# Performance work log

Hardware: AMD Instinct MI355X
Metric: run time of the kernel (lower is better)

## Reference

```python
import jax, jax.numpy as jnp
import numpy as np


def setup_inputs() -> dict:
    key = jax.random.key(0)
    k1, k2, k3, k4, k5 = jax.random.split(key, 5)
    B, S, IN, OUT = 4, 2048, 4096, 4096
    x = jax.random.normal(k1, (B, S, IN), dtype=jnp.float32)
    # int8-style quantized weight stored as int32 values in [0, 255]
    weight_q = jax.random.randint(k2, (OUT, IN), 0, 255, dtype=jnp.int32)
    weight_zero_point = jax.random.randint(k3, (OUT,), 0, 255, dtype=jnp.int32)
    weight_scale = jax.random.uniform(k4, (OUT,), dtype=jnp.float32) * 0.01 + 1e-4
    bias = jax.random.normal(k5, (OUT,), dtype=jnp.float32)
    return {"x": x, "weight_q": weight_q, "weight_zero_point": weight_zero_point,
            "weight_scale": weight_scale, "bias": bias}


def reference(x, weight_q, weight_zero_point, weight_scale, bias):
    # Decompress (dequantize) the weight: per-output-channel affine int8 quantization
    # w_fp = (w_q - zero_point) * scale   -> shape [out, in]
    w = (weight_q - weight_zero_point[:, None]).astype(jnp.float32) * weight_scale[:, None]
    # F.linear: y = x @ w.T + bias
    return jnp.einsum('bsi,oi->bso', x, w) + bias
```

## Files before the change

kernel.cpp:

```cpp
#include <hip/hip_runtime.h>
#include <hip/hip_bf16.h>
#include <stdint.h>

typedef __attribute__((ext_vector_type(4))) int i32x4;

#define K_TOT 4096
#define N_TOT 4096

__global__ __launch_bounds__(512) void quant_x_kernel(const float4* __restrict__ x4,
                                                      unsigned int* __restrict__ xq_dw,
                                                      float* __restrict__ s_row,
                                                      int* __restrict__ qsum_row) {
    const int wave = threadIdx.x >> 6, lane = threadIdx.x & 63;
    const long row = (long)blockIdx.x * 8 + wave;
    const float4* xr = x4 + row * (K_TOT / 4);

    float4 v[16];
    float amax = 0.f;
#pragma unroll
    for (int i = 0; i < 16; ++i) {
        v[i] = xr[lane + i * 64];
        amax = fmaxf(amax, fmaxf(fmaxf(fabsf(v[i].x), fabsf(v[i].y)),
                                 fmaxf(fabsf(v[i].z), fabsf(v[i].w))));
    }
#pragma unroll
    for (int off = 32; off; off >>= 1) amax = fmaxf(amax, __shfl_xor(amax, off));
    amax = fmaxf(amax, 1e-30f);
    const float inv = 127.0f / amax;

    int qsum = 0;
    unsigned int* out = xq_dw + row * (K_TOT / 4);
#pragma unroll
    for (int i = 0; i < 16; ++i) {
        int q0 = (int)rintf(v[i].x * inv), q1 = (int)rintf(v[i].y * inv);
        int q2 = (int)rintf(v[i].z * inv), q3 = (int)rintf(v[i].w * inv);
        qsum += q0 + q1 + q2 + q3;
        out[lane + i * 64] = (unsigned int)(q0 & 255) | ((unsigned int)(q1 & 255) << 8) |
                             ((unsigned int)(q2 & 255) << 16) | ((unsigned int)(q3 & 255) << 24);
    }
#pragma unroll
    for (int off = 32; off; off >>= 1) qsum += __shfl_xor(qsum, off);
    if (lane == 0) { s_row[row] = amax / 127.0f; qsum_row[row] = qsum; }
}

__global__ void pack_w_kernel(const int4* __restrict__ wq, unsigned int* __restrict__ w8) {
    const long o = blockIdx.x;
    const int4* src = wq + o * (K_TOT / 4);
    unsigned int* dst = w8 + o * (K_TOT / 4);
    for (int t = threadIdx.x; t < K_TOT / 4; t += blockDim.x) {
        int4 q = src[t];
        dst[t] = (unsigned int)((q.x - 128) & 255) | ((unsigned int)((q.y - 128) & 255) << 8) |
                 ((unsigned int)((q.z - 128) & 255) << 16) | ((unsigned int)((q.w - 128) & 255) << 24);
    }
}


template<int MH>
__device__ __forceinline__ void read_a8(i32x4 (&a)[4], const char* Ab, int wr, int fr, int kg) {
    const int sw = (fr >> 1) & 3;
#pragma unroll
    for (int mi = 0; mi < 4; ++mi) {
        const int row = wr * 128 + (MH * 4 + mi) * 16 + fr;
        a[mi] = *(const i32x4*)(Ab + row * 64 + ((kg ^ sw) << 4));
    }
}

template<int NH>
__device__ __forceinline__ void read_b8(i32x4 (&b)[2], const char* Bb, int rb, int fr, int kg) {
    const int sw = (fr >> 1) & 3;
#pragma unroll
    for (int ni = 0; ni < 2; ++ni) {
        const int row = rb + (NH * 2 + ni) * 16 + fr;
        b[ni] = *(const i32x4*)(Bb + row * 64 + ((kg ^ sw) << 4));
    }
}

template<int MH, int NH>
__device__ __forceinline__ void mfma8(i32x4 (&acc)[8][4], i32x4 (&a)[4], i32x4 (&b)[2]) {
    __builtin_amdgcn_s_setprio(1);
#pragma unroll
    for (int mi = 0; mi < 4; ++mi)
#pragma unroll
        for (int ni = 0; ni < 2; ++ni)
            acc[MH * 4 + mi][NH * 2 + ni] = __builtin_amdgcn_mfma_i32_16x16x64_i8(
                a[mi], b[ni], acc[MH * 4 + mi][NH * 2 + ni], 0, 0, 0);
    __builtin_amdgcn_s_setprio(0);
}

#define BAR() __builtin_amdgcn_s_barrier()
#define LGKM0() asm volatile("s_waitcnt lgkmcnt(0)" ::: "memory")
#define VMCNT2() asm volatile("s_waitcnt vmcnt(2)" ::: "memory")
#define VMCNT0() asm volatile("s_waitcnt vmcnt(0)" ::: "memory")

__launch_bounds__(512, 2)
__global__ void gemm256_i8_kernel(const char* __restrict__ Aq,
                                  const char* __restrict__ Bq,
                                  const float* __restrict__ s_row,
                                  const int* __restrict__ qsum_row,
                                  const float* __restrict__ scale,
                                  const int* __restrict__ zp,
                                  const float* __restrict__ bias,
                                  float* __restrict__ C) {
    __shared__ __align__(16) char lds[4][256 * 64];

    const int nbn = N_TOT / 256;
    int bid = blockIdx.x;
    const int nwg = gridDim.x;
    if ((nwg & 7) == 0) {
        const int cpx = nwg >> 3;
        bid = (bid & 7) * cpx + (bid >> 3);
    }
    const int bm = bid / nbn, bn = bid % nbn;

    const int tid = threadIdx.x;
    const int w = tid >> 6, lane = tid & 63;
    const int wr = w >> 2, wc = w & 3;
    const int fr = lane & 15, kg = lane >> 4;
    const int brb = (wc >> 1) * 128 + (wc & 1) * 64;

    const long a_row0 = (long)bm * 256;
    const long b_row0 = (long)bn * 256;

    i32x4 acc[8][4] = {};
    i32x4 afr[4], b0[2], b1[2];

    auto stage = [&](int t, int mat, int half) {
        const char* G = (mat == 0) ? Aq : Bq;
        const long row0 = ((mat == 0) ? a_row0 : b_row0) + half * 128;
        char* lb = &lds[(t & 1) * 2 + mat][half * 8192 + w * 1024];
        const int row = w * 16 + (lane >> 2);
        const int c = (lane & 3) ^ (((half * 128 + row) >> 1) & 3);
        const char* g = G + (row0 + row) * K_TOT + (long)t * 64 + c * 16;
        __builtin_amdgcn_global_load_lds(
            (const __attribute__((address_space(1))) void*)g,
            (__attribute__((address_space(3))) void*)lb, 16, 0, 0);
    };

    const char* Ab0 = &lds[0][0];
    const char* Bb0 = &lds[1][0];
    const char* Ab1 = &lds[2][0];
    const char* Bb1 = &lds[3][0];

    stage(0, 0, 0); stage(0, 0, 1); stage(0, 1, 0); stage(0, 1, 1);
    stage(1, 1, 0); stage(1, 1, 1);
    VMCNT2();
    BAR();

    const int NIT = K_TOT / 128;
#pragma unroll 1
    for (int it = 0; it < NIT; ++it) {
        const bool nl = (it != NIT - 1);
        const int t1 = 2 * it + 1, t2 = 2 * it + 2, t3 = 2 * it + 3;

        read_a8<0>(afr, Ab0, wr, fr, kg);
        read_b8<0>(b0, Bb0, brb, fr, kg);
        stage(t1, 0, 0);
        BAR(); LGKM0();
        mfma8<0, 0>(acc, afr, b0);
        BAR();
        read_b8<1>(b1, Bb0, brb, fr, kg);
        stage(t1, 0, 1);
        BAR(); LGKM0();
        mfma8<0, 1>(acc, afr, b1);
        BAR();
        read_a8<1>(afr, Ab0, wr, fr, kg);
        if (nl) stage(t2, 1, 0);
        BAR(); LGKM0();
        mfma8<1, 1>(acc, afr, b1);
        BAR();
        if (nl) stage(t2, 1, 1);
        BAR();
        mfma8<1, 0>(acc, afr, b0);
        if (nl) { VMCNT2(); } else { VMCNT0(); }
        BAR();

        read_a8<0>(afr, Ab1, wr, fr, kg);
        read_b8<0>(b0, Bb1, brb, fr, kg);
        if (nl) stage(t2, 0, 0);
        BAR(); LGKM0();
        mfma8<0, 0>(acc, afr, b0);
        BAR();
        read_b8<1>(b1, Bb1, brb, fr, kg);
        if (nl) stage(t2, 0, 1);
        BAR(); LGKM0();
        mfma8<0, 1>(acc, afr, b1);
        BAR();
        read_a8<1>(afr, Ab1, wr, fr, kg);
        if (nl) stage(t3, 1, 0);
        BAR(); LGKM0();
        mfma8<1, 1>(acc, afr, b1);
        BAR();
        if (nl) stage(t3, 1, 1);
        BAR();
        mfma8<1, 0>(acc, afr, b0);
        if (nl) { VMCNT2(); }
        BAR();
    }

    float scs[4], c1s[4], bbs[4]; int cols[4];
#pragma unroll
    for (int n = 0; n < 4; ++n) {
        cols[n] = (int)b_row0 + wc * 64 + n * 16 + fr;
        scs[n] = scale[cols[n]];
        c1s[n] = (float)(128 - zp[cols[n]]);
        bbs[n] = bias[cols[n]];
    }
#pragma unroll
    for (int m = 0; m < 8; ++m) {
#pragma unroll
        for (int j = 0; j < 4; ++j) {
            const long r = a_row0 + wr * 128 + m * 16 + kg * 4 + j;
            const float sr = s_row[r];
            const float qs = (float)qsum_row[r];
#pragma unroll
            for (int n = 0; n < 4; ++n)
                C[r * N_TOT + cols[n]] = ((float)acc[m][n][j] + c1s[n] * qs) * (scs[n] * sr) + bbs[n];
        }
    }
}

__global__ void fallback_kernel(const float* __restrict__ x, const int* __restrict__ wq,
                                const int* __restrict__ zp, const float* __restrict__ sc,
                                const float* __restrict__ bs, float* __restrict__ y) {
    __shared__ float xs[32][33];
    __shared__ float ws[32][33];
    int bm = blockIdx.y, bn = blockIdx.x;
    int tid = threadIdx.x;
    int r = tid >> 5, c = tid & 31;
    float acc[4] = {0.f, 0.f, 0.f, 0.f};
    for (int k0 = 0; k0 < K_TOT; k0 += 32) {
        for (int t = tid; t < 32 * 32; t += 256) {
            int rr = t >> 5, cc = t & 31;
            xs[rr][cc] = x[(long)(bm * 32 + rr) * K_TOT + k0 + cc];
            int o = bn * 32 + rr;
            ws[rr][cc] = (float)(wq[(long)o * K_TOT + k0 + cc] - zp[o]);
        }
        __syncthreads();
#pragma unroll
        for (int kk = 0; kk < 32; ++kk) {
            float wv = ws[c][kk];
#pragma unroll
            for (int j = 0; j < 4; ++j) acc[j] += xs[r + 8 * j][kk] * wv;
        }
        __syncthreads();
    }
    int o = bn * 32 + c;
    float s = sc[o], b = bs[o];
#pragma unroll
    for (int j = 0; j < 4; ++j)
        y[(long)(bm * 32 + r + 8 * j) * N_TOT + o] = acc[j] * s + b;
}

extern "C" void kernel_launch(void* const* d_in, const int* in_sizes, int n_in,
                              void* d_out, int out_size, void* d_ws, size_t ws_size,
                              hipStream_t stream) {
    const float* x = (const float*)d_in[0];
    const int* wq = (const int*)d_in[1];
    const int* zp = (const int*)d_in[2];
    const float* sc = (const float*)d_in[3];
    const float* bs = (const float*)d_in[4];
    float* y = (float*)d_out;

    const long M = (long)in_sizes[0] / K_TOT;

    size_t xq_bytes = (size_t)M * K_TOT;
    size_t w8_bytes = (size_t)N_TOT * K_TOT;
    size_t s_bytes = (size_t)M * 4;
    size_t q_bytes = (size_t)M * 4;
    size_t need = xq_bytes + w8_bytes + s_bytes + q_bytes + 256;

    if (ws_size >= need && (M & 255) == 0) {
        char* p = (char*)d_ws;
        char* xq = p;                       p += xq_bytes;
        char* w8 = p;                       p += w8_bytes;
        float* s_row = (float*)p;           p += s_bytes;
        int* qsum_row = (int*)p;

        quant_x_kernel<<<(unsigned)(M / 8), 512, 0, stream>>>(
            (const float4*)x, (unsigned int*)xq, s_row, qsum_row);
        pack_w_kernel<<<N_TOT, 256, 0, stream>>>((const int4*)wq, (unsigned int*)w8);

        dim3 grid((unsigned)((M / 256) * (N_TOT / 256)));
        gemm256_i8_kernel<<<grid, 512, 0, stream>>>(
            xq, w8, s_row, qsum_row, sc, zp, bs, y);
    } else {
        dim3 grid(N_TOT / 32, (unsigned)(M / 32));
        fallback_kernel<<<grid, 256, 0, stream>>>(x, wq, zp, sc, bs, y);
    }
}
```

Baseline: 197.5 us.

## Fuse x-quant and weight-pack kernels; coarsen GEMM main-loop phases

Merges the activation quantization and weight packing into one launch, with block ranges split by index, so one launch and its tail are removed. In the int8 GEMM main loop, each half-tile now issues two B-fragment reads and two stage loads together, then runs 16 MFMAs per barrier-delimited phase instead of 8. This halves the barriers and LGKM waits per K step. It holds more B fragments live at once and changes how load issue interleaves with MFMA work, which may raise register pressure and alter latency hiding.

After: 193.6 us. About the same (-1.9%).

```diff
diff --git a/kernel.cpp b/kernel.cpp
--- a/kernel.cpp
+++ b/kernel.cpp
@@ -7,50 +7,53 @@
 #define K_TOT 4096
 #define N_TOT 4096
 
-__global__ __launch_bounds__(512) void quant_x_kernel(const float4* __restrict__ x4,
-                                                      unsigned int* __restrict__ xq_dw,
-                                                      float* __restrict__ s_row,
-                                                      int* __restrict__ qsum_row) {
+__global__ __launch_bounds__(512) void prep_kernel(const float4* __restrict__ x4,
+                                                   unsigned int* __restrict__ xq_dw,
+                                                   float* __restrict__ s_row,
+                                                   int* __restrict__ qsum_row,
+                                                   const int4* __restrict__ wq,
+                                                   unsigned int* __restrict__ w8,
+                                                   int nqb) {
     const int wave = threadIdx.x >> 6, lane = threadIdx.x & 63;
-    const long row = (long)blockIdx.x * 8 + wave;
-    const float4* xr = x4 + row * (K_TOT / 4);
-
-    float4 v[16];
-    float amax = 0.f;
-#pragma unroll
-    for (int i = 0; i < 16; ++i) {
-        v[i] = xr[lane + i * 64];
-        amax = fmaxf(amax, fmaxf(fmaxf(fabsf(v[i].x), fabsf(v[i].y)),
-                                 fmaxf(fabsf(v[i].z), fabsf(v[i].w))));
-    }
-#pragma unroll
-    for (int off = 32; off; off >>= 1) amax = fmaxf(amax, __shfl_xor(amax, off));
-    amax = fmaxf(amax, 1e-30f);
-    const float inv = 127.0f / amax;
-
-    int qsum = 0;
-    unsigned int* out = xq_dw + row * (K_TOT / 4);
-#pragma unroll
-    for (int i = 0; i < 16; ++i) {
-        int q0 = (int)rintf(v[i].x * inv), q1 = (int)rintf(v[i].y * inv);
-        int q2 = (int)rintf(v[i].z * inv), q3 = (int)rintf(v[i].w * inv);
-        qsum += q0 + q1 + q2 + q3;
-        out[lane + i * 64] = (unsigned int)(q0 & 255) | ((unsigned int)(q1 & 255) << 8) |
-                             ((unsigned int)(q2 & 255) << 16) | ((unsigned int)(q3 & 255) << 24);
-    }
-#pragma unroll
-    for (int off = 32; off; off >>= 1) qsum += __shfl_xor(qsum, off);
-    if (lane == 0) { s_row[row] = amax / 127.0f; qsum_row[row] = qsum; }
-}
-
-__global__ void pack_w_kernel(const int4* __restrict__ wq, unsigned int* __restrict__ w8) {
-    const long o = blockIdx.x;
-    const int4* src = wq + o * (K_TOT / 4);
-    unsigned int* dst = w8 + o * (K_TOT / 4);
-    for (int t = threadIdx.x; t < K_TOT / 4; t += blockDim.x) {
-        int4 q = src[t];
-        dst[t] = (unsigned int)((q.x - 128) & 255) | ((unsigned int)((q.y - 128) & 255) << 8) |
-                 ((unsigned int)((q.z - 128) & 255) << 16) | ((unsigned int)((q.w - 128) & 255) << 24);
+    if ((int)blockIdx.x < nqb) {
+        const long row = (long)blockIdx.x * 8 + wave;
+        const float4* xr = x4 + row * (K_TOT / 4);
+        float4 v[16];
+        float amax = 0.f;
+#pragma unroll
+        for (int i = 0; i < 16; ++i) {
+            v[i] = xr[lane + i * 64];
+            amax = fmaxf(amax, fmaxf(fmaxf(fabsf(v[i].x), fabsf(v[i].y)),
+                                     fmaxf(fabsf(v[i].z), fabsf(v[i].w))));
+        }
+#pragma unroll
+        for (int off = 32; off; off >>= 1) amax = fmaxf(amax, __shfl_xor(amax, off));
+        amax = fmaxf(amax, 1e-30f);
+        const float inv = 127.0f / amax;
+        int qsum = 0;
+        unsigned int* out = xq_dw + row * (K_TOT / 4);
+#pragma unroll
+        for (int i = 0; i < 16; ++i) {
+            int q0 = (int)rintf(v[i].x * inv), q1 = (int)rintf(v[i].y * inv);
+            int q2 = (int)rintf(v[i].z * inv), q3 = (int)rintf(v[i].w * inv);
+            qsum += q0 + q1 + q2 + q3;
+            out[lane + i * 64] = (unsigned int)(q0 & 255) | ((unsigned int)(q1 & 255) << 8) |
+                                 ((unsigned int)(q2 & 255) << 16) | ((unsigned int)(q3 & 255) << 24);
+        }
+#pragma unroll
+        for (int off = 32; off; off >>= 1) qsum += __shfl_xor(qsum, off);
+        if (lane == 0) { s_row[row] = amax / 127.0f; qsum_row[row] = qsum; }
+    } else {
+        const long o = (long)((int)blockIdx.x - nqb) * 8 + wave;
+        const int4* src = wq + o * (K_TOT / 4);
+        unsigned int* dst = w8 + o * (K_TOT / 4);
+#pragma unroll
+        for (int i = 0; i < 16; ++i) {
+            int4 q = src[lane + i * 64];
+            dst[lane + i * 64] =
+                (unsigned int)((q.x - 128) & 255) | ((unsigned int)((q.y - 128) & 255) << 8) |
+                ((unsigned int)((q.z - 128) & 255) << 16) | ((unsigned int)((q.w - 128) & 255) << 24);
+        }
     }
 }
 
@@ -77,20 +80,20 @@
 
 template<int MH, int NH>
 __device__ __forceinline__ void mfma8(i32x4 (&acc)[8][4], i32x4 (&a)[4], i32x4 (&b)[2]) {
-    __builtin_amdgcn_s_setprio(1);
 #pragma unroll
     for (int mi = 0; mi < 4; ++mi)
 #pragma unroll
         for (int ni = 0; ni < 2; ++ni)
             acc[MH * 4 + mi][NH * 2 + ni] = __builtin_amdgcn_mfma_i32_16x16x64_i8(
                 a[mi], b[ni], acc[MH * 4 + mi][NH * 2 + ni], 0, 0, 0);
-    __builtin_amdgcn_s_setprio(0);
 }
 
 #define BAR() __builtin_amdgcn_s_barrier()
 #define LGKM0() asm volatile("s_waitcnt lgkmcnt(0)" ::: "memory")
 #define VMCNT2() asm volatile("s_waitcnt vmcnt(2)" ::: "memory")
 #define VMCNT0() asm volatile("s_waitcnt vmcnt(0)" ::: "memory")
+#define PRIO1() __builtin_amdgcn_s_setprio(1)
+#define PRIO0() __builtin_amdgcn_s_setprio(0)
 
 __launch_bounds__(512, 2)
 __global__ void gemm256_i8_kernel(const char* __restrict__ Aq,
@@ -154,45 +157,28 @@
 
         read_a8<0>(afr, Ab0, wr, fr, kg);
         read_b8<0>(b0, Bb0, brb, fr, kg);
-        stage(t1, 0, 0);
-        BAR(); LGKM0();
-        mfma8<0, 0>(acc, afr, b0);
-        BAR();
         read_b8<1>(b1, Bb0, brb, fr, kg);
-        stage(t1, 0, 1);
-        BAR(); LGKM0();
-        mfma8<0, 1>(acc, afr, b1);
+        stage(t1, 0, 0); stage(t1, 0, 1);
+        BAR(); LGKM0();
+        PRIO1(); mfma8<0, 0>(acc, afr, b0); mfma8<0, 1>(acc, afr, b1); PRIO0();
         BAR();
         read_a8<1>(afr, Ab0, wr, fr, kg);
-        if (nl) stage(t2, 1, 0);
-        BAR(); LGKM0();
-        mfma8<1, 1>(acc, afr, b1);
-        BAR();
-        if (nl) stage(t2, 1, 1);
-        BAR();
-        mfma8<1, 0>(acc, afr, b0);
+        if (nl) { stage(t2, 1, 0); stage(t2, 1, 1); }
+        BAR(); LGKM0();
+        PRIO1(); mfma8<1, 1>(acc, afr, b1); mfma8<1, 0>(acc, afr, b0); PRIO0();
         if (nl) { VMCNT2(); } else { VMCNT0(); }
         BAR();
-
         read_a8<0>(afr, Ab1, wr, fr, kg);
         read_b8<0>(b0, Bb1, brb, fr, kg);
-        if (nl) stage(t2, 0, 0);
-        BAR(); LGKM0();
-        mfma8<0, 0>(acc, afr, b0);
-        BAR();
         read_b8<1>(b1, Bb1, brb, fr, kg);
-        if (nl) stage(t2, 0, 1);
-        BAR(); LGKM0();
-        mfma8<0, 1>(acc, afr, b1);
+        if (nl) { stage(t2, 0, 0); stage(t2, 0, 1); }
+        BAR(); LGKM0();
+        PRIO1(); mfma8<0, 0>(acc, afr, b0); mfma8<0, 1>(acc, afr, b1); PRIO0();
         BAR();
         read_a8<1>(afr, Ab1, wr, fr, kg);
-        if (nl) stage(t3, 1, 0);
-        BAR(); LGKM0();
-        mfma8<1, 1>(acc, afr, b1);
-        BAR();
-        if (nl) stage(t3, 1, 1);
-        BAR();
-        mfma8<1, 0>(acc, afr, b0);
+        if (nl) { stage(t3, 1, 0); stage(t3, 1, 1); }
+        BAR(); LGKM0();
+        PRIO1(); mfma8<1, 1>(acc, afr, b1); mfma8<1, 0>(acc, afr, b0); PRIO0();
         if (nl) { VMCNT2(); }
         BAR();
     }
@@ -276,9 +262,11 @@
         float* s_row = (float*)p;           p += s_bytes;
         int* qsum_row = (int*)p;
 
-        quant_x_kernel<<<(unsigned)(M / 8), 512, 0, stream>>>(
-            (const float4*)x, (unsigned int*)xq, s_row, qsum_row);
-        pack_w_kernel<<<N_TOT, 256, 0, stream>>>((const int4*)wq, (unsigned int*)w8);
+        const int nqb = (int)(M / 8);
+        const int npb = N_TOT / 8;
+        prep_kernel<<<nqb + npb, 512, 0, stream>>>(
+            (const float4*)x, (unsigned int*)xq, s_row, qsum_row,
+            (const int4*)wq, (unsigned int*)w8, nqb);
 
         dim3 grid((unsigned)((M / 256) * (N_TOT / 256)));
         gemm256_i8_kernel<<<grid, 512, 0, stream>>>(
```
